# Optimization experiments

Hardware: AMD Instinct MI355X
Metric: run time of the kernel (lower is better)

Reference implementation:

```python
import jax, jax.numpy as jnp
import numpy as np

V, E, H, Z, K = 51, 64, 256, 32, 1000  # vocab, emb, gru hidden, latent, codebook entries
B, T = 2048, 64
COMMIT_W, QUANT_W = 0.1, 0.2


def gru(x_seq, h0, w_ih, w_hh, b_ih, b_hh):
    """torch nn.GRU (1 layer, batch_first). x_seq: (B,T,D), h0: (B,H).
    Returns (outs (B,T,H), h_last (B,H))."""
    xp = jnp.einsum('btd,gd->btg', x_seq, w_ih) + b_ih  # (B,T,3H), precompute input proj

    def step(h, xp_t):
        hp = h @ w_hh.T + b_hh
        xr, xz, xn = jnp.split(xp_t, 3, axis=-1)
        hr, hz, hn = jnp.split(hp, 3, axis=-1)
        r = jax.nn.sigmoid(xr + hr)
        zg = jax.nn.sigmoid(xz + hz)
        n = jnp.tanh(xn + r * hn)
        h_new = (1.0 - zg) * n + zg * h
        return h_new, h_new

    h_last, outs = jax.lax.scan(step, h0, jnp.swapaxes(xp, 0, 1))
    return jnp.swapaxes(outs, 0, 1), h_last


def setup_inputs() -> dict:
    key = jax.random.key(0)
    ks = jax.random.split(key, 16)
    def n(k, shape, s=0.05):
        return (jax.random.normal(k, shape, dtype=jnp.float32) * s).astype(jnp.float32)
    z32 = lambda *s: jnp.zeros(s, jnp.float32)
    return {
        'x': jax.random.randint(ks[0], (B, T), 0, V, dtype=jnp.int32),
        'enc_emb': n(ks[1], (V, E)),
        'enc_wih': n(ks[2], (3 * H, E)),
        'enc_whh': n(ks[3], (3 * H, H)),
        'enc_bih': z32(3 * H), 'enc_bhh': z32(3 * H),
        'w_mu': n(ks[4], (Z, H)), 'b_mu': z32(Z),
        'w_std': n(ks[5], (Z, H)), 'b_std': z32(Z),
        'w_q': n(ks[6], (Z, H)), 'b_q': z32(Z),
        'w_up': n(ks[7], (H, 2 * Z)), 'b_up': z32(H),
        'codebook': jax.random.uniform(ks[8], (K, Z), jnp.float32, -1.0 / K, 1.0 / K),
        'dec_emb': n(ks[9], (V, E)),
        'dec_wih': n(ks[10], (3 * H, E + 2 * Z)),
        'dec_whh': n(ks[11], (3 * H, H)),
        'dec_bih': z32(3 * H), 'dec_bhh': z32(3 * H),
        'w_out': n(ks[12], (V, H)), 'b_out': z32(V),
    }


def reference(x, enc_emb, enc_wih, enc_whh, enc_bih, enc_bhh,
              w_mu, b_mu, w_std, b_std, w_q, b_q, w_up, b_up, codebook,
              dec_emb, dec_wih, dec_whh, dec_bih, dec_bhh, w_out, b_out):
    # ---- Encoder (dropout p=0.0; eval mode) ----
    emb = enc_emb[x]                                    # (B,T,E)
    h0 = jnp.zeros((x.shape[0], H), emb.dtype)
    _, h_last = gru(emb, h0, enc_wih, enc_whh, enc_bih, enc_bhh)  # (B,H)
    mu = h_last @ w_mu.T + b_mu                         # (B,Z)
    logvar = h_last @ w_std.T + b_std
    toq = h_last @ w_q.T + b_q
    KL = jnp.sum(0.5 * (mu ** 2 + jnp.exp(logvar) - logvar - 1.0))
    z = mu  # module overrides sampled z with mu

    # ---- Vector quantization (codebook nearest neighbor) ----
    d = (jnp.sum(toq ** 2, -1, keepdims=True)
         + jnp.sum(codebook ** 2, -1)
         - 2.0 * toq @ codebook.T)                      # (B,K)
    idx = jnp.argmin(d, axis=-1)                        # (B,)
    q = codebook[idx]                                   # (B,Z)
    commitment = jnp.mean((jax.lax.stop_gradient(q) - toq) ** 2, axis=-1)
    embedding = jnp.mean((q - jax.lax.stop_gradient(toq)) ** 2, axis=-1)
    Q = jnp.sum(commitment * COMMIT_W + embedding * QUANT_W)
    q_st = toq + jax.lax.stop_gradient(q - toq)         # straight-through

    # ---- Decoder ----
    zcat = jnp.concatenate([q_st, z], axis=-1)          # (B,2Z)
    hidden = zcat @ w_up.T + b_up                       # (B,H)
    src, tgt = x[:, :-1], x[:, 1:]
    z_rep = jnp.broadcast_to(zcat[:, None, :], (x.shape[0], src.shape[1], 2 * Z))
    dec_in = jnp.concatenate([z_rep, dec_emb[src]], axis=-1)  # (B,T-1,2Z+E)
    outs, _ = gru(dec_in, hidden, dec_wih, dec_whh, dec_bih, dec_bhh)  # (B,T-1,H)
    logits = outs @ w_out.T + b_out                     # (B,T-1,V)

    logp = jax.nn.log_softmax(logits, axis=-1)
    tok_lp = jnp.take_along_axis(logp, tgt[..., None], axis=-1)[..., 0]
    mask = tgt != 0  # CrossEntropyLoss ignore_index=0, reduction='sum'
    xloss = -jnp.sum(jnp.where(mask, tok_lp, 0.0))
    nonpadded = jnp.sum(mask)
    pred_tokens = jnp.argmax(logits, axis=-1)
    return xloss, nonpadded, pred_tokens, KL, Q, idx[:, None]
```

## Files before the change

kernel.cpp:

```cpp
#include <hip/hip_runtime.h>
#include <hip/hip_bf16.h>

#define B_ 2048
#define T_ 64
#define H_ 256
#define V_ 51
#define Z_ 32
#define K_ 1000
#define LOG2E 1.4426950408889634f

typedef __bf16 bf16x8 __attribute__((ext_vector_type(8)));
typedef float floatx4 __attribute__((ext_vector_type(4)));

__device__ inline unsigned short f2bf(float f){
    unsigned int u = __float_as_uint(f);
    u += 0x7fffu + ((u >> 16) & 1u);
    return (unsigned short)(u >> 16);
}
__device__ inline float sigm2(float x){
    float e; asm("v_exp_f32 %0, -%1" : "=v"(e) : "v"(x));
    return __builtin_amdgcn_rcpf(1.0f + e);
}
__device__ inline float tanh2(float y){
    float t = y * (-2.0f*LOG2E);
    float e; asm("v_exp_f32 %0, %1" : "=v"(e) : "v"(t));
    return __builtin_fmaf(2.0f, __builtin_amdgcn_rcpf(1.0f + e), -1.0f);
}
__device__ inline float permlane_merge(float d, float s){
    asm("v_permlane32_swap_b32 %0, %1" : "+v"(d), "+v"(s));
    return d;
}
__device__ inline unsigned int cvtpk_bf16(float lo, float hi){
    unsigned int r;
    asm("v_cvt_pk_bf16_f32 %0, %1, %2" : "=v"(r) : "v"(lo), "v"(hi));
    return r;
}
__device__ inline float lo16(unsigned int u){ return __uint_as_float(u << 16); }
__device__ inline float hi16(unsigned int u){ return __uint_as_float(u & 0xffff0000u); }

#define TBLE  78336
#define PACKE 471552
#define OUTE  487936
#define PROJE 512512
#define MIDE  578048
#define CNE   579048

__global__ __launch_bounds__(256) void k_prep(
    const float* __restrict__ enc_emb, const float* __restrict__ enc_wih, const float* __restrict__ enc_bih,
    const float* __restrict__ enc_bhh,
    const float* __restrict__ dec_emb, const float* __restrict__ dec_wih, const float* __restrict__ dec_bih,
    const float* __restrict__ dec_bhh,
    const float* __restrict__ whh_e, const float* __restrict__ whh_d, const float* __restrict__ w_out,
    const float* __restrict__ w_mu, const float* __restrict__ w_std, const float* __restrict__ w_q,
    const float* __restrict__ w_up, const float* __restrict__ cb,
    unsigned short* __restrict__ tep, unsigned short* __restrict__ tdp,
    unsigned short* __restrict__ bpe, unsigned short* __restrict__ bpd,
    unsigned short* __restrict__ bpo,
    float* __restrict__ wTproj, float* __restrict__ wTmid, float* __restrict__ cnorm)
{
    int id = blockIdx.x*256 + threadIdx.x;
    if (id < TBLE){
        int which = id / (V_*768), r = id % (V_*768);
        int v = r / 768, g = r % 768;
        int gate = g >> 8, col = g & 255;
        float s;
        if (!which){
            s = enc_bih[g] + (gate < 2 ? enc_bhh[g] : 0.0f);
            for (int e=0;e<64;++e) s += enc_emb[v*64+e]*enc_wih[g*64+e];
            if (gate < 2) s *= LOG2E;
            tep[(v*256+col)*4 + gate] = f2bf(s);
        } else {
            s = dec_bih[g] + (gate < 2 ? dec_bhh[g] : 0.0f);
            for (int e=0;e<64;++e) s += dec_emb[v*64+e]*dec_wih[g*128+64+e];
            if (gate < 2) s *= LOG2E;
            tdp[(v*256+col)*4 + gate] = f2bf(s);
        }
    } else if (id < PACKE){
        int rid = id - TBLE;
        int which = rid / 196608, e = rid % 196608;
        int j = e & 7, lane = (e>>3)&63, kt = (e>>9)&7, nt = e>>12;
        int k = kt*32 + (lane>>4)*8 + j, n = nt*16 + (lane&15);
        const float* wmat = which ? whh_d : whh_e;
        float wv = wmat[n*256+k];
        if (nt < 32) wv *= LOG2E;
        (which ? bpd : bpe)[e] = f2bf(wv);
    } else if (id < OUTE){
        int cid = id - PACKE;
        int j = cid & 7, lane = (cid>>3)&63, kt = (cid>>9)&7, nt = cid>>12;
        int k = kt*32 + (lane>>4)*8 + j, n = nt*16 + (lane&15);
        bpo[cid] = f2bf(n < V_ ? w_out[n*256+k] : 0.0f);
    } else if (id < PROJE){
        int e = id - OUTE;
        int k = e / 96, o = e % 96;
        float v = (o < 32) ? w_mu[o*H_+k] : (o < 64 ? w_std[(o-32)*H_+k] : w_q[(o-64)*H_+k]);
        wTproj[e] = v;
    } else if (id < MIDE){
        int e = id - PROJE;
        int k = e >> 10, o = e & 1023;
        float v;
        if (o < 256) v = w_up[o*64+k];
        else {
            int g = o - 256;
            v = dec_wih[(size_t)g*128 + k];
            if (g < 512) v *= LOG2E;
        }
        wTmid[e] = v;
    } else if (id < CNE){
        int k = id - MIDE;
        float s = 0.f;
        const float* cv = cb + (size_t)k*Z_;
        for (int ci=0;ci<Z_;++ci) s = __builtin_fmaf(cv[ci],cv[ci],s);
        cnorm[k] = s;
    }
}

template<int DEC>
__global__ __launch_bounds__(512, 2) void k_gru(
    const int* __restrict__ x, const unsigned short* __restrict__ tblg,
    const unsigned short* __restrict__ bpack, const float* __restrict__ bhh,
    const float* __restrict__ h0, const unsigned short* __restrict__ zvp,
    float* __restrict__ h_last, unsigned short* __restrict__ outs)
{
    const int Tn = DEC ? (T_-1) : T_;
    __shared__ alignas(16) unsigned short tbl[V_*1024];
    __shared__ alignas(16) unsigned short hbuf[2*4096];
    __shared__ unsigned int tpk[T_][2];

    const int tid = threadIdx.x;
    const int w = tid>>6, lane = tid&63, lr = lane&15, lp = lane>>4;
    const int b0 = blockIdx.x*8;
    const int jm = w + ((lane>=32)?8:0);
    const int col_m = jm*16 + lr;
    const int rbase = (lp&1)*4;
    const int colm4 = col_m*4;

    const bf16x8* bp = (const bf16x8*)bpack;
    bf16x8 wf[2][3][8];
    #pragma unroll
    for (int ji=0; ji<2; ++ji)
      #pragma unroll
      for (int g=0; g<3; ++g)
        #pragma unroll
        for (int kt=0; kt<8; ++kt)
            wf[ji][g][kt] = bp[(((g*16) + w + 8*ji)*8 + kt)*64 + lane];

    {
        uint4* d4 = (uint4*)tbl; const uint4* s4 = (const uint4*)tblg;
        for (int i=tid; i<(V_*1024)/8; i+=512) d4[i] = s4[i];
    }
    for (int i=tid; i<4096; i+=512){
        int bufi = i>>11, rr = 8 + ((i>>8)&7), c = i&255;
        hbuf[bufi*4096 + rr*256 + c] = 0;
    }
    if (tid < 128){
        int t = tid>>1, g = tid&1;
        unsigned int p = 0;
        #pragma unroll
        for (int r=0;r<4;++r) p |= ((unsigned int)x[(size_t)(b0 + g*4 + r)*T_ + t]) << (8*r);
        tpk[t][g] = p;
    }

    const float bhn = bhh[2*H_ + col_m];
    float hreg[4];
    int waddr[4];
    #pragma unroll
    for (int q=0; q<4; ++q){
        int row = rbase + q;
        float hv = DEC ? h0[(size_t)(b0+row)*H_ + col_m] : 0.0f;
        hreg[q] = hv;
        waddr[q] = row*256 + (col_m ^ (row<<3));
        hbuf[waddr[q]] = f2bf(hv);
    }
    float zr_[4], zz_[4], zn_[4];
    if (DEC){
        #pragma unroll
        for (int q=0; q<4; ++q){
            const unsigned short* zp = zvp + (((size_t)(b0+rbase+q))*256 + col_m)*4;
            uint2 zv = *(const uint2*)zp;
            zr_[q] = lo16(zv.x); zz_[q] = hi16(zv.x); zn_[q] = lo16(zv.y);
        }
    }
    const int s3 = (lr&7)<<3, lpb = lp*8;
    const int aidx0 = lr*256 + (lpb ^ s3);
    const int aidx1 = lr*256 + ((32 + lpb) ^ s3);
    const int crow = w, cc4 = lane<<2;
    const int csrc = crow*256 + (cc4 ^ (crow<<3));
    unsigned short* cdst0 = DEC ? (outs + ((size_t)(b0+crow)*(T_-1))*H_ + cc4) : nullptr;
    __syncthreads();

#define LDH(i) (*(const bf16x8*)&hbuf[(cur<<12) + (i)])
#define MFMA_(ji,g,kt,av) acc[ji][g] = __builtin_amdgcn_mfma_f32_16x16x32_bf16(av, wf[ji][g][kt], acc[ji][g], 0,0,0)

    auto step = [&](int t, int cur) {
        const int nxt = cur^1;
        unsigned int tp = tpk[t][lp&1];
        floatx4 acc[2][3] = {};

        bf16x8 a[8];
        #pragma unroll
        for (int kt=0; kt<8; ++kt)
            a[kt] = LDH(((kt&1)?aidx1:aidx0) + ((kt>>1)<<6));

        uint2 tv[4];
        #pragma unroll
        for (int q=0;q<4;++q){
            int tok = (tp >> (8*q)) & 255;
            tv[q] = *(const uint2*)&tbl[(tok<<10) + colm4];
        }

        #pragma unroll
        for (int kt=0; kt<8; ++kt){
            MFMA_(0,0,kt,a[kt]); MFMA_(1,0,kt,a[kt]);
            MFMA_(0,1,kt,a[kt]); MFMA_(1,1,kt,a[kt]);
            MFMA_(0,2,kt,a[kt]); MFMA_(1,2,kt,a[kt]);
        }

        float rg[4], zg[4], hv[4];
        #pragma unroll
        for (int q=0;q<4;++q){
            float rm = permlane_merge(acc[0][0][q], acc[1][0][q]);
            float xr = lo16(tv[q].x); if (DEC) xr += zr_[q];
            rg[q] = sigm2(xr + rm);
        }
        #pragma unroll
        for (int q=0;q<4;++q){
            float zm = permlane_merge(acc[0][1][q], acc[1][1][q]);
            float xz = hi16(tv[q].x); if (DEC) xz += zz_[q];
            zg[q] = sigm2(xz + zm);
        }
        #pragma unroll
        for (int q=0;q<4;++q){
            float nm = permlane_merge(acc[0][2][q], acc[1][2][q]);
            float xn = lo16(tv[q].y); if (DEC) xn += zn_[q];
            float ng = tanh2(__builtin_fmaf(rg[q], nm + bhn, xn));
            hv[q] = __builtin_fmaf(zg[q], hreg[q] - ng, ng);
            hreg[q] = hv[q];
        }
        unsigned int p01 = cvtpk_bf16(hv[0], hv[1]);
        unsigned int p23 = cvtpk_bf16(hv[2], hv[3]);
        hbuf[(nxt<<12) + waddr[0]] = (unsigned short)p01;
        hbuf[(nxt<<12) + waddr[1]] = (unsigned short)(p01 >> 16);
        hbuf[(nxt<<12) + waddr[2]] = (unsigned short)p23;
        hbuf[(nxt<<12) + waddr[3]] = (unsigned short)(p23 >> 16);
        __syncthreads();
        if (DEC){
            uint2 v = *(const uint2*)&hbuf[(nxt<<12) + csrc];
            *(uint2*)(cdst0 + (size_t)t*H_) = v;
        }
    };

    for (int t=0; t+1<Tn; t+=2){ step(t,0); step(t+1,1); }
    if (Tn & 1) step(Tn-1, 0);

#undef LDH
#undef MFMA_

    if (!DEC){
        #pragma unroll
        for (int q=0; q<4; ++q)
            h_last[(size_t)(b0+rbase+q)*H_ + col_m] = hreg[q];
    }
}

__global__ __launch_bounds__(256) void k_latmid(
    const float* __restrict__ hlast,
    const float* __restrict__ b_mu, const float* __restrict__ b_std, const float* __restrict__ b_q,
    const float* __restrict__ cb, const float* __restrict__ cnorm,
    const float* __restrict__ wTproj, const float* __restrict__ wTmid,
    const float* __restrict__ b_up,
    float* __restrict__ hidden, unsigned short* __restrict__ zvp,
    float* __restrict__ pKL, float* __restrict__ pQ, float* __restrict__ out_idx)
{
    __shared__ float hs[H_];
    __shared__ float pp[2][96];
    __shared__ float pout[96];
    __shared__ float zsl[64];
    __shared__ float rbuf[8];
    __shared__ int   ribuf[8];
    __shared__ int   kbc;
    const int tid = threadIdx.x;
    const int b = blockIdx.x;

    hs[tid] = hlast[(size_t)b*H_ + tid];
    __syncthreads();

    if (tid < 192){
        int o = tid % 96, kh = tid / 96;
        const float* wp = wTproj + kh*128*96 + o;
        const float* hp = hs + kh*128;
        float s = 0.f;
        #pragma unroll 8
        for (int k=0;k<128;++k) s = __builtin_fmaf(hp[k], wp[k*96], s);
        pp[kh][o] = s;
    }
    __syncthreads();
    if (tid < 96){
        float bias = (tid<32) ? b_mu[tid] : (tid<64 ? b_std[tid-32] : b_q[tid-64]);
        pout[tid] = pp[0][tid] + pp[1][tid] + bias;
    }
    __syncthreads();

    if (tid < 32){
        float m = pout[tid], l = pout[32+tid];
        float kl = 0.5f*(m*m + __expf(l) - l - 1.0f);
        #pragma unroll
        for (int off=16; off>0; off>>=1) kl += __shfl_down(kl, off, 32);
        if (tid==0) pKL[b] = kl;
    }

    const float* tq = pout + 64;
    float bd = 3.4e38f; int bk = K_;
    #pragma unroll
    for (int c4 = 0; c4 < 4; ++c4){
        int k = tid + c4*256;
        if (k < K_){
            const float4* cr = (const float4*)(cb + (size_t)k*Z_);
            float dot = 0.f;
            #pragma unroll
            for (int j=0;j<8;++j){
                float4 cv = cr[j];
                dot = __builtin_fmaf(cv.x, tq[j*4+0], dot);
                dot = __builtin_fmaf(cv.y, tq[j*4+1], dot);
                dot = __builtin_fmaf(cv.z, tq[j*4+2], dot);
                dot = __builtin_fmaf(cv.w, tq[j*4+3], dot);
            }
            float d = cnorm[k] - 2.0f*dot;
            if (d < bd){ bd = d; bk = k; }
        }
    }
    #pragma unroll
    for (int off=32; off>0; off>>=1){
        float od = __shfl_down(bd, off, 64);
        int   ok = __shfl_down(bk, off, 64);
        if (od < bd || (od == bd && ok < bk)){ bd = od; bk = ok; }
    }
    if ((tid&63)==0){ rbuf[tid>>6] = bd; ribuf[tid>>6] = bk; }
    __syncthreads();
    if (tid==0){
        float fb = rbuf[0]; int fk = ribuf[0];
        for (int wv=1; wv<4; ++wv)
            if (rbuf[wv] < fb || (rbuf[wv]==fb && ribuf[wv]<fk)){ fb=rbuf[wv]; fk=ribuf[wv]; }
        kbc = fk;
        out_idx[b] = (float)fk;
        float s = 0.f;
        const float* cv = cb + (size_t)fk*Z_;
        for (int ci=0;ci<Z_;++ci){ float df = cv[ci]-tq[ci]; s = __builtin_fmaf(df,df,s); }
        pQ[b] = s*(0.3f/32.0f);
    }
    __syncthreads();
    const int ksel = kbc;
    if (tid < 64) zsl[tid] = (tid < Z_) ? cb[(size_t)ksel*Z_ + tid] : pout[tid-Z_];
    __syncthreads();

    float a0=0.f, a1=0.f, a2=0.f, a3=0.f;
    const float* wm = wTmid + tid;
    #pragma unroll 8
    for (int k=0;k<64;++k){
        float zk = zsl[k];
        const float* wr = wm + k*1024;
        a0 = __builtin_fmaf(zk, wr[0],   a0);
        a1 = __builtin_fmaf(zk, wr[256], a1);
        a2 = __builtin_fmaf(zk, wr[512], a2);
        a3 = __builtin_fmaf(zk, wr[768], a3);
    }
    hidden[(size_t)b*H_ + tid] = a0 + b_up[tid];
    unsigned int lo = ((unsigned int)f2bf(a2) << 16) | (unsigned int)f2bf(a1);
    unsigned int hi = (unsigned int)f2bf(a3);
    *(uint2*)(zvp + ((size_t)b*256 + tid)*4) = make_uint2(lo, hi);
}

__global__ __launch_bounds__(256) void k_loss(
    const unsigned short* __restrict__ outs, const unsigned short* __restrict__ bpo,
    const float* __restrict__ b_out, const int* __restrict__ x,
    float* __restrict__ pred, float* __restrict__ pXL, float* __restrict__ pNP)
{
    __shared__ float ll[16][64];
    __shared__ float bo[64];
    __shared__ float redf[256], redn[256];
    const int tid = threadIdx.x, w = tid>>6, lane = tid&63, lr = lane&15, lp = lane>>4;
    const bf16x8* bpofr = (const bf16x8*)bpo;
    bf16x8 bw[8];
    #pragma unroll
    for (int kt=0;kt<8;++kt) bw[kt] = bpofr[(w*8+kt)*64 + lane];
    if (tid < 64) bo[tid] = (tid < V_) ? b_out[tid] : 0.0f;
    float xl = 0.f, npn = 0.f;
    const int row = tid>>4, vl = tid&15;
    for (int cc=0; cc<4; ++cc){
        int row0 = (blockIdx.x*4 + cc)*16;
        floatx4 acc = {0,0,0,0};
        #pragma unroll
        for (int kt=0;kt<8;++kt){
            bf16x8 av = *(const bf16x8*)&outs[(size_t)(row0+lr)*H_ + kt*32 + lp*8];
            acc = __builtin_amdgcn_mfma_f32_16x16x32_bf16(av, bw[kt], acc, 0,0,0);
        }
        __syncthreads();
        #pragma unroll
        for (int q=0;q<4;++q) ll[lp*4+q][w*16+lr] = acc[q];
        __syncthreads();
        float lv[4];
        #pragma unroll
        for (int k2=0;k2<4;++k2){
            int v = vl + 16*k2;
            lv[k2] = (v < V_) ? ll[row][v] + bo[v] : -3.4e38f;
        }
        float m = lv[0]; int am = vl;
        #pragma unroll
        for (int k2=1;k2<4;++k2){ if (lv[k2] > m){ m = lv[k2]; am = vl + 16*k2; } }
        #pragma unroll
        for (int off=1; off<16; off<<=1){
            float om = __shfl_xor(m, off, 16);
            int oa = __shfl_xor(am, off, 16);
            if (om > m || (om == m && oa < am)){ m = om; am = oa; }
        }
        float se = 0.f;
        #pragma unroll
        for (int k2=0;k2<4;++k2) se += __expf(lv[k2]-m);
        #pragma unroll
        for (int off=1; off<16; off<<=1) se += __shfl_xor(se, off, 16);
        if (vl == 0){
            int rowg = row0 + row;
            int b = rowg/63, tt = rowg - b*63;
            int tgt = x[(size_t)b*T_ + tt + 1];
            pred[rowg] = (float)am;
            if (tgt != 0){
                float lse = m + __logf(se);
                xl += ll[row][tgt] + bo[tgt] - lse;
                npn += 1.f;
            }
        }
    }
    redf[tid]=xl; redn[tid]=npn;
    __syncthreads();
    for (int s=128;s>0;s>>=1){ if (tid<s){ redf[tid]+=redf[tid+s]; redn[tid]+=redn[tid+s]; } __syncthreads(); }
    if (tid==0){ pXL[blockIdx.x]=redf[0]; pNP[blockIdx.x]=redn[0]; }
}

__global__ __launch_bounds__(256) void k_reduce(
    const float* __restrict__ pKL, const float* __restrict__ pQ,
    const float* __restrict__ pXL, const float* __restrict__ pNP, float* __restrict__ dout)
{
    __shared__ float r[256];
    const int tid = threadIdx.x;
    float a = 0.f;
    for (int i=tid;i<2048;i+=256) a += pKL[i];
    r[tid] = a; __syncthreads();
    for (int s=128;s>0;s>>=1){ if (tid<s) r[tid]+=r[tid+s]; __syncthreads(); }
    if (tid==0) dout[129026] = r[0];
    __syncthreads();
    a = 0.f;
    for (int i=tid;i<2048;i+=256) a += pQ[i];
    r[tid] = a; __syncthreads();
    for (int s=128;s>0;s>>=1){ if (tid<s) r[tid]+=r[tid+s]; __syncthreads(); }
    if (tid==0) dout[129027] = r[0];
    __syncthreads();
    a = 0.f;
    for (int i=tid;i<2016;i+=256) a += pXL[i];
    r[tid] = a; __syncthreads();
    for (int s=128;s>0;s>>=1){ if (tid<s) r[tid]+=r[tid+s]; __syncthreads(); }
    if (tid==0) dout[0] = -r[0];
    __syncthreads();
    a = 0.f;
    for (int i=tid;i<2016;i+=256) a += pNP[i];
    r[tid] = a; __syncthreads();
    for (int s=128;s>0;s>>=1){ if (tid<s) r[tid]+=r[tid+s]; __syncthreads(); }
    if (tid==0) dout[1] = r[0];
}

extern "C" void kernel_launch(void* const* d_in, const int* in_sizes, int n_in,
                              void* d_out, int out_size, void* d_ws, size_t ws_size,
                              hipStream_t stream)
{
    const int*   x       = (const int*)  d_in[0];
    const float* enc_emb = (const float*)d_in[1];
    const float* enc_wih = (const float*)d_in[2];
    const float* enc_whh = (const float*)d_in[3];
    const float* enc_bih = (const float*)d_in[4];
    const float* enc_bhh = (const float*)d_in[5];
    const float* w_mu    = (const float*)d_in[6];
    const float* b_mu    = (const float*)d_in[7];
    const float* w_std   = (const float*)d_in[8];
    const float* b_std   = (const float*)d_in[9];
    const float* w_q     = (const float*)d_in[10];
    const float* b_q     = (const float*)d_in[11];
    const float* w_up    = (const float*)d_in[12];
    const float* b_up    = (const float*)d_in[13];
    const float* cb      = (const float*)d_in[14];
    const float* dec_emb = (const float*)d_in[15];
    const float* dec_wih = (const float*)d_in[16];
    const float* dec_whh = (const float*)d_in[17];
    const float* dec_bih = (const float*)d_in[18];
    const float* dec_bhh = (const float*)d_in[19];
    const float* w_out   = (const float*)d_in[20];
    const float* b_out   = (const float*)d_in[21];

    float* ws = (float*)d_ws;
    unsigned short* tep = (unsigned short*)(ws + 0);
    unsigned short* tdp = (unsigned short*)(ws + 26112);
    unsigned short* bpe = (unsigned short*)(ws + 52224);
    unsigned short* bpd = (unsigned short*)(ws + 150528);
    unsigned short* bpo = (unsigned short*)(ws + 248832);
    float* hl   = ws + 257024;
    float* wTproj = ws + 781312;
    float* wTmid  = ws + 805888;
    float* cnorm  = ws + 871424;
    float* hid  = ws + 912384;
    unsigned short* zvp  = (unsigned short*)(ws + 1436672);
    unsigned short* outs = (unsigned short*)(ws + 2485248);
    float* pKL  = ws + 19000320;
    float* pQ   = ws + 19002368;
    float* pXL  = ws + 19004416;
    float* pNP  = ws + 19006432;

    float* dout = (float*)d_out;

    k_prep<<<2262,256,0,stream>>>(enc_emb, enc_wih, enc_bih, enc_bhh,
                                  dec_emb, dec_wih, dec_bih, dec_bhh,
                                  enc_whh, dec_whh, w_out,
                                  w_mu, w_std, w_q, w_up, cb,
                                  tep, tdp, bpe, bpd, bpo,
                                  wTproj, wTmid, cnorm);
    k_gru<0><<<256,512,0,stream>>>(x, tep, bpe, enc_bhh, nullptr, nullptr, hl, nullptr);
    k_latmid<<<2048,256,0,stream>>>(hl, b_mu, b_std, b_q, cb, cnorm, wTproj, wTmid, b_up,
                                    hid, zvp, pKL, pQ, dout + 129028);
    k_gru<1><<<256,512,0,stream>>>(x, tdp, bpd, dec_bhh, hid, zvp, nullptr, outs);
    k_loss<<<2016,256,0,stream>>>(outs, bpo, b_out, x, dout + 2, pXL, pNP);
    k_reduce<<<1,256,0,stream>>>(pKL, pQ, pXL, pNP, dout);
}
```

Measured before the change: 284.5 us.

## Split GRU step MFMAs to overlap r/z gate math with n-gate matmul

The recurrent step now issues the r and z gate MFMAs first, computes the sigmoid gates, and only then issues the n-gate MFMAs, separated by a sched_barrier and wrapped in s_setprio. The goal is to hide transcendental and permlane latency behind matrix work on the serial recurrence path. It also vectorizes the prep kernel's 64-element embedding dot products with float4 loads. The volatile permlane and sched_barrier restrict compiler scheduling, which could serialize work instead of overlapping it.

```diff
diff --git a/kernel.cpp b/kernel.cpp
--- a/kernel.cpp
+++ b/kernel.cpp
@@ -30,6 +30,10 @@
     asm("v_permlane32_swap_b32 %0, %1" : "+v"(d), "+v"(s));
     return d;
 }
+__device__ inline float permlane_merge_v(float d, float s){
+    asm volatile("v_permlane32_swap_b32 %0, %1" : "+v"(d), "+v"(s));
+    return d;
+}
 __device__ inline unsigned int cvtpk_bf16(float lo, float hi){
     unsigned int r;
     asm("v_cvt_pk_bf16_f32 %0, %1, %2" : "=v"(r) : "v"(lo), "v"(hi));
@@ -44,6 +48,17 @@
 #define PROJE 512512
 #define MIDE  578048
 #define CNE   579048
+
+__device__ inline float dot64_f4(const float4* a, const float4* b){
+    float s = 0.f;
+    #pragma unroll
+    for (int i=0;i<16;++i){
+        float4 x = a[i], y = b[i];
+        s = __builtin_fmaf(x.x,y.x,s); s = __builtin_fmaf(x.y,y.y,s);
+        s = __builtin_fmaf(x.z,y.z,s); s = __builtin_fmaf(x.w,y.w,s);
+    }
+    return s;
+}
 
 __global__ __launch_bounds__(256) void k_prep(
     const float* __restrict__ enc_emb, const float* __restrict__ enc_wih, const float* __restrict__ enc_bih,
@@ -66,12 +81,12 @@
         float s;
         if (!which){
             s = enc_bih[g] + (gate < 2 ? enc_bhh[g] : 0.0f);
-            for (int e=0;e<64;++e) s += enc_emb[v*64+e]*enc_wih[g*64+e];
+            s += dot64_f4((const float4*)(enc_emb + v*64), (const float4*)(enc_wih + g*64));
             if (gate < 2) s *= LOG2E;
             tep[(v*256+col)*4 + gate] = f2bf(s);
         } else {
             s = dec_bih[g] + (gate < 2 ? dec_bhh[g] : 0.0f);
-            for (int e=0;e<64;++e) s += dec_emb[v*64+e]*dec_wih[g*128+64+e];
+            s += dot64_f4((const float4*)(dec_emb + v*64), (const float4*)(dec_wih + g*128 + 64));
             if (gate < 2) s *= LOG2E;
             tdp[(v*256+col)*4 + gate] = f2bf(s);
         }
@@ -208,26 +223,32 @@
             tv[q] = *(const uint2*)&tbl[(tok<<10) + colm4];
         }
 
+        __builtin_amdgcn_s_setprio(1);
         #pragma unroll
         for (int kt=0; kt<8; ++kt){
             MFMA_(0,0,kt,a[kt]); MFMA_(1,0,kt,a[kt]);
             MFMA_(0,1,kt,a[kt]); MFMA_(1,1,kt,a[kt]);
-            MFMA_(0,2,kt,a[kt]); MFMA_(1,2,kt,a[kt]);
-        }
-
-        float rg[4], zg[4], hv[4];
+        }
+        __builtin_amdgcn_s_setprio(0);
+
+        float rg[4], zg[4];
         #pragma unroll
         for (int q=0;q<4;++q){
-            float rm = permlane_merge(acc[0][0][q], acc[1][0][q]);
+            float rm = permlane_merge_v(acc[0][0][q], acc[1][0][q]);
             float xr = lo16(tv[q].x); if (DEC) xr += zr_[q];
             rg[q] = sigm2(xr + rm);
-        }
-        #pragma unroll
-        for (int q=0;q<4;++q){
-            float zm = permlane_merge(acc[0][1][q], acc[1][1][q]);
+            float zm = permlane_merge_v(acc[0][1][q], acc[1][1][q]);
             float xz = hi16(tv[q].x); if (DEC) xz += zz_[q];
             zg[q] = sigm2(xz + zm);
         }
+        __builtin_amdgcn_sched_barrier(0);
+
+        __builtin_amdgcn_s_setprio(1);
+        #pragma unroll
+        for (int kt=0; kt<8; ++kt){ MFMA_(0,2,kt,a[kt]); MFMA_(1,2,kt,a[kt]); }
+        __builtin_amdgcn_s_setprio(0);
+
+        float hv[4];
         #pragma unroll
         for (int q=0;q<4;++q){
             float nm = permlane_merge(acc[0][2][q], acc[1][2][q]);
```

After: 433.1 us. 1.52x slower.
